# Kernel optimization log

Hardware: AMD Instinct MI355X
Metric: run time of the kernel (lower is better)

The kernel has to match this reference:

```python
import jax, jax.numpy as jnp
import numpy as np

B, S, D, H, DK = 8, 1024, 1024, 16, 64
DV = D // H  # 64


def setup_inputs() -> dict:
    key = jax.random.key(0)
    ks = jax.random.split(key, 9)
    s = 1.0 / np.sqrt(D)
    return {
        "x": jax.random.normal(ks[0], (B, S, D), dtype=jnp.float32),
        "masks": jnp.ones((B, S), dtype=jnp.int32),
        "Wq": jax.random.normal(ks[1], (D, H * DK), dtype=jnp.float32) * s,
        "bq": jnp.zeros((H * DK,), dtype=jnp.float32),
        "Wk": jax.random.normal(ks[2], (D, H * DK), dtype=jnp.float32) * s,
        "bk": jnp.zeros((H * DK,), dtype=jnp.float32),
        "Wv": jax.random.normal(ks[3], (D, H * DV), dtype=jnp.float32) * s,
        "bv": jnp.zeros((H * DV,), dtype=jnp.float32),
        "Wo": jax.random.normal(ks[4], (H * DV, D), dtype=jnp.float32) * s,
        "bo": jnpp_zeros() if False else jnp.zeros((D,), dtype=jnp.float32),
    }


def reference(x, masks, Wq, bq, Wk, bk, Wv, bv, Wo, bo):
    # projections -> [B, H, S, d]
    q = (x @ Wq + bq).reshape(B, S, H, DK).transpose(0, 2, 1, 3)
    k = (x @ Wk + bk).reshape(B, S, H, DK).transpose(0, 2, 1, 3)
    v = (x @ Wv + bv).reshape(B, S, H, DV).transpose(0, 2, 1, 3)
    # scaled dot-product attention with padding mask
    logits = jnp.einsum('bhqd,bhkd->bhqk', q, k) / jnp.sqrt(jnp.float32(DK))
    mask = masks[:, None, None, :]  # [B,1,1,S]
    logits = jnp.where(mask == 0, jnp.float32(-1e9), logits)
    scores = jax.nn.softmax(logits, axis=-1)
    out = jnp.einsum('bhqk,bhkd->bhqd', scores, v)
    out = out.transpose(0, 2, 1, 3).reshape(B, S, H * DV)
    # output projection; dropout is identity in eval mode
    return out @ Wo + bo
```

## Files before the change

### kernel.cpp

```cpp
#include <hip/hip_runtime.h>
#include <stdint.h>

#define B_ 8
#define S_ 1024
#define D_ 1024
#define H_ 16
#define DK_ 64
#define DV_ 64

typedef __attribute__((ext_vector_type(8))) short short8;
typedef __attribute__((ext_vector_type(4))) float f32x4;

__device__ __forceinline__ unsigned short f2bf(float f) {
  union { float f; unsigned u; } v; v.f = f;
  return (unsigned short)((v.u + 0x7fffu + ((v.u >> 16) & 1u)) >> 16);
}
__device__ __forceinline__ unsigned short f2bf_trunc(float f) {
  union { float f; unsigned u; } v; v.f = f;
  return (unsigned short)(v.u >> 16);
}

__device__ __forceinline__ void ld_lds16(const unsigned short* g, unsigned short* l) {
  __builtin_amdgcn_global_load_lds((const __attribute__((address_space(1))) void*)g,
                                   (__attribute__((address_space(3))) void*)l, 16, 0, 0);
}

__global__ __launch_bounds__(256) void prep_kernel(const float* __restrict__ x,
                                                   unsigned short* __restrict__ xb,
                                                   const float* __restrict__ W0,
                                                   const float* __restrict__ W1,
                                                   const float* __restrict__ W2,
                                                   const float* __restrict__ W3,
                                                   unsigned short* __restrict__ T0,
                                                   unsigned short* __restrict__ T1,
                                                   unsigned short* __restrict__ T2,
                                                   unsigned short* __restrict__ T3) {
  const int z = blockIdx.z;
  if (z >= 4) {
    size_t blk = (size_t)(z - 4) * 256 + blockIdx.y * 16 + blockIdx.x;
    size_t i = (blk * 256 + threadIdx.x) * 4;
    float4 v = *(const float4*)(x + i);
    ushort4 o;
    o.x = f2bf(v.x); o.y = f2bf(v.y); o.z = f2bf(v.z); o.w = f2bf(v.w);
    *(ushort4*)(xb + i) = o;
    return;
  }
  __shared__ __align__(16) unsigned short tl[64][65];
  const float* W; unsigned short* Wt;
  switch (z) {
    case 0: W = W0; Wt = T0; break;
    case 1: W = W1; Wt = T1; break;
    case 2: W = W2; Wt = T2; break;
    default: W = W3; Wt = T3; break;
  }
  const int xx = threadIdx.x & 63;
  const int y4 = threadIdx.x >> 6;
  const int bn = blockIdx.x * 64;
  const int bk = blockIdx.y * 64;
  #pragma unroll
  for (int r = y4; r < 64; r += 4)
    tl[r][xx] = f2bf(W[(size_t)(bk + r) * 1024 + bn + xx]);
  __syncthreads();
  #pragma unroll
  for (int r = y4; r < 64; r += 4)
    Wt[(size_t)(bn + r) * 1024 + bk + xx] = tl[xx][r];
}


struct SJob { const unsigned short* g; unsigned short* l; };

__device__ __forceinline__ void stage128(const unsigned short* __restrict__ G,
                                         unsigned short* __restrict__ L, int t) {
  #pragma unroll
  for (int i = 0; i < 2; i++) {
    int s = i * 512 + t;
    int r = s >> 3, cb = s & 7;
    int c = cb ^ (r & 7);
    ld_lds16(G + (size_t)r * 1024 + c * 8, L + (size_t)s * 8);
  }
}

template <bool SW>
__device__ __forceinline__ f32x4 MM(short8 a, short8 b, f32x4 c) {
  if constexpr (SW) return __builtin_amdgcn_mfma_f32_16x16x32_bf16(b, a, c, 0, 0, 0);
  else              return __builtin_amdgcn_mfma_f32_16x16x32_bf16(a, b, c, 0, 0, 0);
}

template <bool SW, int VM>
__device__ __forceinline__ void ktile2(const unsigned short* __restrict__ As_,
                                       const unsigned short* __restrict__ Bs_,
                                       f32x4 (&acc)[4][4],
                                       SJob a0, SJob a1, SJob b2,
                                       int t, int wm, int wn, int l15, int quad, int l7) {
  const int cb0 = (quad ^ l7) * 8;
  const int cb1 = ((4 | quad) ^ l7) * 8;
  short8 af[4], bf[4];

  #pragma unroll
  for (int mi = 0; mi < 4; mi++)
    af[mi] = *(const short8*)&As_[(wm + mi * 16 + l15) * 64 + cb0];
  #pragma unroll
  for (int ni = 0; ni < 4; ni++)
    bf[ni] = *(const short8*)&Bs_[(wn + ni * 16 + l15) * 64 + cb0];
  if (a0.g) stage128(a0.g, a0.l, t);
  if (a1.g) stage128(a1.g, a1.l, t);
  __builtin_amdgcn_s_barrier();
  asm volatile("s_waitcnt lgkmcnt(0)" ::: "memory");
  __builtin_amdgcn_s_setprio(1);
  #pragma unroll
  for (int mi = 0; mi < 4; mi++)
    #pragma unroll
    for (int ni = 0; ni < 4; ni++)
      acc[mi][ni] = MM<SW>(af[mi], bf[ni], acc[mi][ni]);
  __builtin_amdgcn_s_setprio(0);
  __builtin_amdgcn_s_barrier();

  #pragma unroll
  for (int mi = 0; mi < 4; mi++)
    af[mi] = *(const short8*)&As_[(wm + mi * 16 + l15) * 64 + cb1];
  #pragma unroll
  for (int ni = 0; ni < 4; ni++)
    bf[ni] = *(const short8*)&Bs_[(wn + ni * 16 + l15) * 64 + cb1];
  if (b2.g) stage128(b2.g, b2.l, t);
  __builtin_amdgcn_s_barrier();
  asm volatile("s_waitcnt lgkmcnt(0)" ::: "memory");
  __builtin_amdgcn_s_setprio(1);
  #pragma unroll
  for (int mi = 0; mi < 4; mi++)
    #pragma unroll
    for (int ni = 0; ni < 4; ni++)
      acc[mi][ni] = MM<SW>(af[mi], bf[ni], acc[mi][ni]);
  __builtin_amdgcn_s_setprio(0);
  if constexpr (VM == 6) asm volatile("s_waitcnt vmcnt(6)" ::: "memory");
  if constexpr (VM == 0) asm volatile("s_waitcnt vmcnt(0)" ::: "memory");
  __builtin_amdgcn_s_barrier();
}

template <bool SW>
__device__ __forceinline__ void gemm_core(const unsigned short* __restrict__ Ag,
                                          const unsigned short* __restrict__ Bg,
                                          unsigned short* __restrict__ Asl,
                                          unsigned short* __restrict__ Bsl,
                                          f32x4 (&acc)[4][4],
                                          int t, int wm, int wn, int l15, int quad, int l7) {
  unsigned short* A0 = Asl;
  unsigned short* A1 = Asl + 16384;
  unsigned short* A2 = Asl + 32768;
  unsigned short* Bs0 = Bsl;
  unsigned short* Bs1 = Bsl + 8192;
  unsigned short* Bs2 = Bsl + 16384;

  stage128(Ag,                 A0, t);
  stage128(Ag + 128 * 1024,    A0 + 8192, t);
  stage128(Bg,                 Bs0, t);
  stage128(Ag + 64,                A1, t);
  stage128(Ag + 64 + 128 * 1024,   A1 + 8192, t);
  stage128(Bg + 64,                Bs1, t);
  asm volatile("s_waitcnt vmcnt(6)" ::: "memory");
  __builtin_amdgcn_s_barrier();

  #pragma unroll 1
  for (int J = 0; J < 12; J += 3) {
    const unsigned short* Aj = Ag + (size_t)J * 64;
    const unsigned short* Bj = Bg + (size_t)J * 64;
    ktile2<SW, 6>(A0, Bs0, acc,
                  SJob{Aj + 2 * 64, A2}, SJob{Aj + 2 * 64 + 128 * 1024, A2 + 8192},
                  SJob{Bj + 2 * 64, Bs2}, t, wm, wn, l15, quad, l7);
    ktile2<SW, 6>(A1, Bs1, acc,
                  SJob{Aj + 3 * 64, A0}, SJob{Aj + 3 * 64 + 128 * 1024, A0 + 8192},
                  SJob{Bj + 3 * 64, Bs0}, t, wm, wn, l15, quad, l7);
    ktile2<SW, 6>(A2, Bs2, acc,
                  SJob{Aj + 4 * 64, A1}, SJob{Aj + 4 * 64 + 128 * 1024, A1 + 8192},
                  SJob{Bj + 4 * 64, Bs1}, t, wm, wn, l15, quad, l7);
  }
  ktile2<SW, 6>(A0, Bs0, acc,
                SJob{Ag + 14 * 64, A2}, SJob{Ag + 14 * 64 + 128 * 1024, A2 + 8192},
                SJob{Bg + 14 * 64, Bs2}, t, wm, wn, l15, quad, l7);
  ktile2<SW, 6>(A1, Bs1, acc,
                SJob{Ag + 15 * 64, A0}, SJob{Ag + 15 * 64 + 128 * 1024, A0 + 8192},
                SJob{Bg + 15 * 64, Bs0}, t, wm, wn, l15, quad, l7);
  ktile2<SW, 0>(A2, Bs2, acc,
                SJob{nullptr, nullptr}, SJob{nullptr, nullptr}, SJob{nullptr, nullptr},
                t, wm, wn, l15, quad, l7);
  ktile2<SW, -1>(A0, Bs0, acc,
                 SJob{nullptr, nullptr}, SJob{nullptr, nullptr}, SJob{nullptr, nullptr},
                 t, wm, wn, l15, quad, l7);
}

__global__ __launch_bounds__(512, 2) void gemm_qkv8(const unsigned short* __restrict__ A,
                                                    const unsigned short* __restrict__ Bt,
                                                    const float* __restrict__ bq,
                                                    const float* __restrict__ bk,
                                                    const float* __restrict__ bv,
                                                    const int* __restrict__ masks,
                                                    unsigned short* __restrict__ q,
                                                    unsigned short* __restrict__ kk,
                                                    unsigned short* __restrict__ vT) {
  extern __shared__ unsigned short lds[];
  unsigned short* Asl = lds;
  unsigned short* Bsl = lds + 3 * 16384;
  const int t = threadIdx.x;
  const int w = t >> 6, lane = t & 63;
  const int l15 = lane & 15, quad = lane >> 4, l7 = l15 & 7;
  const int lin = blockIdx.y * 24 + blockIdx.x;
  const int lin2 = (lin & 7) * 96 + (lin >> 3);
  const int bxi = lin2 % 24, byi = lin2 / 24;
  const int bm = byi * 256, bn = bxi * 128;
  const int wm = (w >> 1) * 64, wn = (w & 1) * 64;
  const bool vsec = (bxi >= 16);
  const unsigned short* Ag = A + (size_t)bm * 1024;
  const unsigned short* Bg = Bt + (size_t)bn * 1024;

  f32x4 acc[4][4] = {};
  if (!vsec) gemm_core<false>(Ag, Bg, Asl, Bsl, acc, t, wm, wn, l15, quad, l7);
  else       gemm_core<true >(Ag, Bg, Asl, Bsl, acc, t, wm, wn, l15, quad, l7);

  if (!vsec) {
    int sec = bxi >> 3;
    const float* bsel = (sec == 0) ? bq : bk;
    unsigned short* dst = (sec == 0) ? q : kk;
    float scale = (sec == 0) ? 0.180336880f : 1.0f;
    #pragma unroll
    for (int ni = 0; ni < 4; ni++) {
      int c = (bn & 1023) + wn + ni * 16 + l15;
      float bvv = bsel[c];
      int hh = c >> 6, d = c & 63;
      #pragma unroll
      for (int mi = 0; mi < 4; mi++) {
        int row0 = bm + wm + mi * 16 + quad * 4;
        #pragma unroll
        for (int r = 0; r < 4; r++) {
          int row = row0 + r;
          int b = row >> 10, s = row & 1023;
          dst[(((size_t)(b * H_ + hh)) * S_ + s) * DK_ + d] = f2bf((acc[mi][ni][r] + bvv) * scale);
        }
      }
    }
  } else {
    #pragma unroll
    for (int ni = 0; ni < 4; ni++) {
      int cbase = (bn & 1023) + wn + ni * 16;
      #pragma unroll
      for (int mi = 0; mi < 4; mi++) {
        int row = bm + wm + mi * 16 + l15;
        int b = row >> 10, s = row & 1023;
        float mf = (masks[b * S_ + s] != 0) ? 1.0f : 0.0f;
        #pragma unroll
        for (int r = 0; r < 4; r++) {
          int c = cbase + quad * 4 + r;
          int hh = c >> 6, d = c & 63;
          vT[(((size_t)(b * H_ + hh)) * DV_ + d) * S_ + s] = f2bf((acc[mi][ni][r] + bv[c]) * mf);
        }
      }
    }
  }
}

__global__ __launch_bounds__(512, 2) void gemm_out8(const unsigned short* __restrict__ A,
                                                    const unsigned short* __restrict__ Bt,
                                                    const float* __restrict__ bias,
                                                    float* __restrict__ Cout) {
  extern __shared__ unsigned short lds[];
  unsigned short* Asl = lds;
  unsigned short* Bsl = lds + 3 * 16384;
  const int t = threadIdx.x;
  const int w = t >> 6, lane = t & 63;
  const int l15 = lane & 15, quad = lane >> 4, l7 = l15 & 7;
  const int lin = blockIdx.y * 8 + blockIdx.x;
  const int lin2 = (lin & 7) * 32 + (lin >> 3);
  const int bxi = lin2 % 8, byi = lin2 / 8;
  const int bm = byi * 256, bn = bxi * 128;
  const int wm = (w >> 1) * 64, wn = (w & 1) * 64;
  const unsigned short* Ag = A + (size_t)bm * 1024;
  const unsigned short* Bg = Bt + (size_t)bn * 1024;

  f32x4 acc[4][4] = {};
  gemm_core<false>(Ag, Bg, Asl, Bsl, acc, t, wm, wn, l15, quad, l7);

  #pragma unroll
  for (int ni = 0; ni < 4; ni++) {
    int col = bn + wn + ni * 16 + l15;
    float bvv = bias[col];
    #pragma unroll
    for (int mi = 0; mi < 4; mi++) {
      int row0 = bm + wm + mi * 16 + quad * 4;
      #pragma unroll
      for (int r = 0; r < 4; r++)
        Cout[(size_t)(row0 + r) * 1024 + col] = acc[mi][ni][r] + bvv;
    }
  }
}

#define PLD 72
#define VROWS 65
__global__ __launch_bounds__(256) void attn_kernel(const unsigned short* __restrict__ Q,
                                                   const unsigned short* __restrict__ Kb,
                                                   const unsigned short* __restrict__ Vt,
                                                   const int* __restrict__ masks,
                                                   unsigned short* __restrict__ O) {
  __shared__ __align__(16) unsigned short Pl[128 * PLD];
  __shared__ __align__(16) unsigned short Ks[2 * 64 * 64];
  __shared__ __align__(16) unsigned short Vs[(2 * VROWS + 15) * 64];
  const int t = threadIdx.x;
  const int wave = t >> 6, lane = t & 63;
  const int l15 = lane & 15, quad = lane >> 4;
  const int l7 = l15 & 7;
  const int bh = blockIdx.x;
  const int qt = blockIdx.y;
  const int b = bh >> 4, h = bh & 15;

  const unsigned short* Qg = Q + ((size_t)bh * S_ + qt * 128) * DK_;
  const unsigned short* Kg = Kb + (size_t)bh * S_ * DK_;
  const unsigned short* Vg = Vt + (size_t)bh * DV_ * S_;
  const int wslot = (t & ~63);

  int mv[4];
  #pragma unroll
  for (int j = 0; j < 4; j++)
    mv[j] = masks[b * S_ + (j * 4 + wave) * 64 + lane];

  short8 aq[2][2];
  #pragma unroll
  for (int mb = 0; mb < 2; mb++)
    #pragma unroll
    for (int kf = 0; kf < 2; kf++)
      aq[mb][kf] = *(const short8*)(Qg + (size_t)(wave * 32 + mb * 16 + l15) * 64 + kf * 32 + quad * 8);

  auto stage = [&](int kt, int buf) {
    const unsigned short* Kt = Kg + (size_t)kt * 64 * DK_;
    unsigned short* Kd = &Ks[buf * 4096];
    unsigned short* Vd = &Vs[buf * (VROWS * 64)];
    #pragma unroll
    for (int i = 0; i < 2; i++) {
      int p = i * 256 + t;
      int rk = p >> 3, ck = (p & 7) ^ (rk & 7);
      ld_lds16(Kt + (size_t)rk * DK_ + ck * 8, &Kd[(i * 256 + wslot) * 8]);
      ld_lds16(Vg + (size_t)rk * S_ + kt * 64 + ck * 8, &Vd[(i * 256 + wslot) * 8]);
    }
    if (wave == (kt & 3))
      Vd[64 * 64 + lane] = (mv[kt >> 2] != 0) ? (unsigned short)0x3F80 : (unsigned short)0;
  };

  f32x4 o_acc[2][5] = {};

  stage(0, 0);
  __syncthreads();

  #pragma unroll 2
  for (int kt = 0; kt < 16; kt++) {
    const int cur = kt & 1;
    if (kt < 15) stage(kt + 1, cur ^ 1);
    const unsigned short* Kc = &Ks[cur * 4096];
    const unsigned short* Vc = &Vs[cur * (VROWS * 64)];

    f32x4 sc[2][4];
    #pragma unroll
    for (int n = 0; n < 4; n++) {
      short8 bk0 = *(const short8*)&Kc[(n * 16 + l15) * 64 + (quad ^ l7) * 8];
      short8 bk1 = *(const short8*)&Kc[(n * 16 + l15) * 64 + ((4 + quad) ^ l7) * 8];
      #pragma unroll
      for (int mb = 0; mb < 2; mb++) {
        f32x4 c = {};
        c = __builtin_amdgcn_mfma_f32_16x16x32_bf16(bk0, aq[mb][0], c, 0, 0, 0);
        c = __builtin_amdgcn_mfma_f32_16x16x32_bf16(bk1, aq[mb][1], c, 0, 0, 0);
        sc[mb][n] = c;
      }
    }
    #pragma unroll
    for (int mb = 0; mb < 2; mb++)
      #pragma unroll
      for (int n = 0; n < 4; n++) {
        ushort4 pk;
        pk.x = f2bf_trunc(__builtin_amdgcn_exp2f(sc[mb][n][0]));
        pk.y = f2bf_trunc(__builtin_amdgcn_exp2f(sc[mb][n][1]));
        pk.z = f2bf_trunc(__builtin_amdgcn_exp2f(sc[mb][n][2]));
        pk.w = f2bf_trunc(__builtin_amdgcn_exp2f(sc[mb][n][3]));
        *(ushort4*)&Pl[(wave * 32 + mb * 16 + l15) * PLD + n * 16 + quad * 4] = pk;
      }
    #pragma unroll
    for (int kf = 0; kf < 2; kf++) {
      short8 ap[2];
      #pragma unroll
      for (int mb = 0; mb < 2; mb++)
        ap[mb] = *(const short8*)&Pl[(wave * 32 + mb * 16 + l15) * PLD + kf * 32 + quad * 8];
      #pragma unroll
      for (int n = 0; n < 5; n++) {
        short8 bv = *(const short8*)&Vc[(n * 16 + l15) * 64 + ((kf * 4 + quad) ^ l7) * 8];
        #pragma unroll
        for (int mb = 0; mb < 2; mb++)
          o_acc[mb][n] = __builtin_amdgcn_mfma_f32_16x16x32_bf16(ap[mb], bv, o_acc[mb][n], 0, 0, 0);
      }
    }
    __syncthreads();
  }

  #pragma unroll
  for (int mb = 0; mb < 2; mb++)
    #pragma unroll
    for (int r = 0; r < 4; r++) {
      float l = __shfl(o_acc[mb][4][r], lane & 48, 64);
      float inv = __builtin_amdgcn_rcpf(l);
      int qrow = qt * 128 + wave * 32 + mb * 16 + quad * 4 + r;
      #pragma unroll
      for (int n = 0; n < 4; n++) {
        int col = h * 64 + n * 16 + l15;
        O[((size_t)b * S_ + qrow) * D_ + col] = f2bf(o_acc[mb][n][r] * inv);
      }
    }
}

extern "C" void kernel_launch(void* const* d_in, const int* in_sizes, int n_in,
                              void* d_out, int out_size, void* d_ws, size_t ws_size,
                              hipStream_t stream) {
  (void)in_sizes; (void)n_in; (void)out_size; (void)ws_size;
  const float* x  = (const float*)d_in[0];
  const int* masks = (const int*)d_in[1];
  const float* Wq = (const float*)d_in[2];
  const float* bq = (const float*)d_in[3];
  const float* Wk = (const float*)d_in[4];
  const float* bk = (const float*)d_in[5];
  const float* Wv = (const float*)d_in[6];
  const float* bv = (const float*)d_in[7];
  const float* Wo = (const float*)d_in[8];
  const float* bo = (const float*)d_in[9];

  char* p = (char*)d_ws;
  unsigned short* xb    = (unsigned short*)p; p += (size_t)8192 * 1024 * 2;
  unsigned short* WqkvT = (unsigned short*)p; p += (size_t)3072 * 1024 * 2;
  unsigned short* WoT   = (unsigned short*)p; p += (size_t)1024 * 1024 * 2;
  unsigned short* q     = (unsigned short*)p; p += (size_t)8192 * 1024 * 2;
  unsigned short* kk    = (unsigned short*)p; p += (size_t)8192 * 1024 * 2;
  unsigned short* vT    = (unsigned short*)p; p += (size_t)8192 * 1024 * 2;
  unsigned short* at    = (unsigned short*)p; p += (size_t)8192 * 1024 * 2;

  static bool attr_done = false;
  if (!attr_done) {
    hipFuncSetAttribute((const void*)gemm_qkv8, hipFuncAttributeMaxDynamicSharedMemorySize, 147456);
    hipFuncSetAttribute((const void*)gemm_out8, hipFuncAttributeMaxDynamicSharedMemorySize, 147456);
    attr_done = true;
  }

  prep_kernel<<<dim3(16, 16, 36), 256, 0, stream>>>(
      x, xb, Wq, Wk, Wv, Wo,
      WqkvT, WqkvT + (size_t)1024 * 1024, WqkvT + (size_t)2048 * 1024, WoT);
  gemm_qkv8<<<dim3(24, 32), 512, 147456, stream>>>(xb, WqkvT, bq, bk, bv, masks, q, kk, vT);
  attn_kernel<<<dim3(128, 8), 256, 0, stream>>>(q, kk, vT, masks, at);
  gemm_out8<<<dim3(8, 32), 512, 147456, stream>>>(at, WoT, bo, (float*)d_out);
}
```

Before: 249.3 us.

## Use 256x256 tiles with double-buffered pipeline for QKV projection GEMM

Replaces the QKV GEMM's 256x128 tile with a 256x256 tile per block, with eight waves each computing 128x64. It uses a two-stage LDS double buffer and interleaves the global-to-LDS staging into four MFMA sub-phases, with barriers and priority hints between them. The larger tile raises arithmetic intensity and halves the block count (384 blocks), reducing redundant A/B loads. In exchange it needs more accumulator registers at two blocks per CU, exposes more load latency with only two buffers, and drops the block-index swizzle for L2 locality in both GEMMs.

```diff
diff --git a/kernel.cpp b/kernel.cpp
--- a/kernel.cpp
+++ b/kernel.cpp
@@ -66,7 +66,6 @@
     Wt[(size_t)(bn + r) * 1024 + bk + xx] = tl[xx][r];
 }
 
-
 struct SJob { const unsigned short* g; unsigned short* l; };
 
 __device__ __forceinline__ void stage128(const unsigned short* __restrict__ G,
@@ -84,6 +83,208 @@
 __device__ __forceinline__ f32x4 MM(short8 a, short8 b, f32x4 c) {
   if constexpr (SW) return __builtin_amdgcn_mfma_f32_16x16x32_bf16(b, a, c, 0, 0, 0);
   else              return __builtin_amdgcn_mfma_f32_16x16x32_bf16(a, b, c, 0, 0, 0);
+}
+
+template <bool SW, int VM>
+__device__ __forceinline__ void ktile256(const unsigned short* __restrict__ As_,
+                                         const unsigned short* __restrict__ Bs_,
+                                         f32x4 (&acc)[8][4],
+                                         SJob sA0, SJob sA1, SJob sB0, SJob sB1,
+                                         int t, int wm, int wn, int l15, int quad, int l7) {
+  const int cb0 = (quad ^ l7) * 8;
+  const int cb1 = ((4 | quad) ^ l7) * 8;
+  short8 bh0[4], bh1[4];
+  short8 a0, a1, a2, a3;
+
+  #pragma unroll
+  for (int ni = 0; ni < 4; ni++) {
+    bh0[ni] = *(const short8*)&Bs_[(wn + ni * 16 + l15) * 64 + cb0];
+    bh1[ni] = *(const short8*)&Bs_[(wn + ni * 16 + l15) * 64 + cb1];
+  }
+  a0 = *(const short8*)&As_[(wm + 0 * 16 + l15) * 64 + cb0];
+  a1 = *(const short8*)&As_[(wm + 0 * 16 + l15) * 64 + cb1];
+  a2 = *(const short8*)&As_[(wm + 1 * 16 + l15) * 64 + cb0];
+  a3 = *(const short8*)&As_[(wm + 1 * 16 + l15) * 64 + cb1];
+  if (sA0.g) stage128(sA0.g, sA0.l, t);
+  __builtin_amdgcn_s_barrier();
+  asm volatile("s_waitcnt lgkmcnt(0)" ::: "memory");
+  __builtin_amdgcn_s_setprio(1);
+  #pragma unroll
+  for (int ni = 0; ni < 4; ni++) {
+    acc[0][ni] = MM<SW>(a0, bh0[ni], acc[0][ni]);
+    acc[0][ni] = MM<SW>(a1, bh1[ni], acc[0][ni]);
+    acc[1][ni] = MM<SW>(a2, bh0[ni], acc[1][ni]);
+    acc[1][ni] = MM<SW>(a3, bh1[ni], acc[1][ni]);
+  }
+  __builtin_amdgcn_s_setprio(0);
+  __builtin_amdgcn_s_barrier();
+
+  a0 = *(const short8*)&As_[(wm + 2 * 16 + l15) * 64 + cb0];
+  a1 = *(const short8*)&As_[(wm + 2 * 16 + l15) * 64 + cb1];
+  a2 = *(const short8*)&As_[(wm + 3 * 16 + l15) * 64 + cb0];
+  a3 = *(const short8*)&As_[(wm + 3 * 16 + l15) * 64 + cb1];
+  if (sA1.g) stage128(sA1.g, sA1.l, t);
+  __builtin_amdgcn_s_barrier();
+  asm volatile("s_waitcnt lgkmcnt(0)" ::: "memory");
+  __builtin_amdgcn_s_setprio(1);
+  #pragma unroll
+  for (int ni = 0; ni < 4; ni++) {
+    acc[2][ni] = MM<SW>(a0, bh0[ni], acc[2][ni]);
+    acc[2][ni] = MM<SW>(a1, bh1[ni], acc[2][ni]);
+    acc[3][ni] = MM<SW>(a2, bh0[ni], acc[3][ni]);
+    acc[3][ni] = MM<SW>(a3, bh1[ni], acc[3][ni]);
+  }
+  __builtin_amdgcn_s_setprio(0);
+  __builtin_amdgcn_s_barrier();
+
+  a0 = *(const short8*)&As_[(wm + 4 * 16 + l15) * 64 + cb0];
+  a1 = *(const short8*)&As_[(wm + 4 * 16 + l15) * 64 + cb1];
+  a2 = *(const short8*)&As_[(wm + 5 * 16 + l15) * 64 + cb0];
+  a3 = *(const short8*)&As_[(wm + 5 * 16 + l15) * 64 + cb1];
+  if (sB0.g) stage128(sB0.g, sB0.l, t);
+  __builtin_amdgcn_s_barrier();
+  asm volatile("s_waitcnt lgkmcnt(0)" ::: "memory");
+  __builtin_amdgcn_s_setprio(1);
+  #pragma unroll
+  for (int ni = 0; ni < 4; ni++) {
+    acc[4][ni] = MM<SW>(a0, bh0[ni], acc[4][ni]);
+    acc[4][ni] = MM<SW>(a1, bh1[ni], acc[4][ni]);
+    acc[5][ni] = MM<SW>(a2, bh0[ni], acc[5][ni]);
+    acc[5][ni] = MM<SW>(a3, bh1[ni], acc[5][ni]);
+  }
+  __builtin_amdgcn_s_setprio(0);
+  __builtin_amdgcn_s_barrier();
+
+  a0 = *(const short8*)&As_[(wm + 6 * 16 + l15) * 64 + cb0];
+  a1 = *(const short8*)&As_[(wm + 6 * 16 + l15) * 64 + cb1];
+  a2 = *(const short8*)&As_[(wm + 7 * 16 + l15) * 64 + cb0];
+  a3 = *(const short8*)&As_[(wm + 7 * 16 + l15) * 64 + cb1];
+  if (sB1.g) stage128(sB1.g, sB1.l, t);
+  __builtin_amdgcn_s_barrier();
+  asm volatile("s_waitcnt lgkmcnt(0)" ::: "memory");
+  __builtin_amdgcn_s_setprio(1);
+  #pragma unroll
+  for (int ni = 0; ni < 4; ni++) {
+    acc[6][ni] = MM<SW>(a0, bh0[ni], acc[6][ni]);
+    acc[6][ni] = MM<SW>(a1, bh1[ni], acc[6][ni]);
+    acc[7][ni] = MM<SW>(a2, bh0[ni], acc[7][ni]);
+    acc[7][ni] = MM<SW>(a3, bh1[ni], acc[7][ni]);
+  }
+  __builtin_amdgcn_s_setprio(0);
+  if constexpr (VM == 4) asm volatile("s_waitcnt vmcnt(4)" ::: "memory");
+  if constexpr (VM == 0) asm volatile("s_waitcnt vmcnt(0)" ::: "memory");
+  __builtin_amdgcn_s_barrier();
+}
+
+template <bool SW>
+__device__ __forceinline__ void gemm_core256(const unsigned short* __restrict__ Ag,
+                                             const unsigned short* __restrict__ Bg,
+                                             unsigned short* __restrict__ Asl,
+                                             unsigned short* __restrict__ Bsl,
+                                             f32x4 (&acc)[8][4],
+                                             int t, int wm, int wn, int l15, int quad, int l7) {
+  unsigned short* A0 = Asl;
+  unsigned short* A1 = Asl + 16384;
+  unsigned short* B0s = Bsl;
+  unsigned short* B1s = Bsl + 16384;
+
+  stage128(Ag,              A0, t);
+  stage128(Ag + 128 * 1024, A0 + 8192, t);
+  stage128(Bg,              B0s, t);
+  stage128(Bg + 128 * 1024, B0s + 8192, t);
+  stage128(Bg + 64,              B1s, t);
+  stage128(Bg + 64 + 128 * 1024, B1s + 8192, t);
+  asm volatile("s_waitcnt vmcnt(4)" ::: "memory");
+  __builtin_amdgcn_s_barrier();
+
+  #pragma unroll 1
+  for (int J = 0; J < 14; J += 2) {
+    const unsigned short* Aj = Ag + (size_t)J * 64;
+    const unsigned short* Bj = Bg + (size_t)J * 64;
+    ktile256<SW, 4>(A0, B0s, acc,
+                    SJob{Aj + 64, A1}, SJob{Aj + 64 + 128 * 1024, A1 + 8192},
+                    SJob{Bj + 128, B0s}, SJob{Bj + 128 + 128 * 1024, B0s + 8192},
+                    t, wm, wn, l15, quad, l7);
+    ktile256<SW, 4>(A1, B1s, acc,
+                    SJob{Aj + 128, A0}, SJob{Aj + 128 + 128 * 1024, A0 + 8192},
+                    SJob{Bj + 192, B1s}, SJob{Bj + 192 + 128 * 1024, B1s + 8192},
+                    t, wm, wn, l15, quad, l7);
+  }
+  ktile256<SW, 0>(A0, B0s, acc,
+                  SJob{Ag + 15 * 64, A1}, SJob{Ag + 15 * 64 + 128 * 1024, A1 + 8192},
+                  SJob{nullptr, nullptr}, SJob{nullptr, nullptr},
+                  t, wm, wn, l15, quad, l7);
+  ktile256<SW, -1>(A1, B1s, acc,
+                   SJob{nullptr, nullptr}, SJob{nullptr, nullptr},
+                   SJob{nullptr, nullptr}, SJob{nullptr, nullptr},
+                   t, wm, wn, l15, quad, l7);
+}
+
+__global__ __launch_bounds__(512, 2) void gemm_qkv8(const unsigned short* __restrict__ A,
+                                                    const unsigned short* __restrict__ Bt,
+                                                    const float* __restrict__ bq,
+                                                    const float* __restrict__ bk,
+                                                    const float* __restrict__ bv,
+                                                    const int* __restrict__ masks,
+                                                    unsigned short* __restrict__ q,
+                                                    unsigned short* __restrict__ kk,
+                                                    unsigned short* __restrict__ vT) {
+  extern __shared__ unsigned short lds[];
+  unsigned short* Asl = lds;
+  unsigned short* Bsl = lds + 2 * 16384;
+  const int t = threadIdx.x;
+  const int w = t >> 6, lane = t & 63;
+  const int l15 = lane & 15, quad = lane >> 4, l7 = l15 & 7;
+  const int bxi = blockIdx.x, byi = blockIdx.y;
+  const int bm = byi * 256, bn = bxi * 256;
+  const int wm = (w >> 2) * 128, wn = (w & 3) * 64;
+  const bool vsec = (bxi >= 8);
+  const unsigned short* Ag = A + (size_t)bm * 1024;
+  const unsigned short* Bg = Bt + (size_t)bn * 1024;
+
+  f32x4 acc[8][4] = {};
+  if (!vsec) gemm_core256<false>(Ag, Bg, Asl, Bsl, acc, t, wm, wn, l15, quad, l7);
+  else       gemm_core256<true >(Ag, Bg, Asl, Bsl, acc, t, wm, wn, l15, quad, l7);
+
+  if (!vsec) {
+    int sec = bxi >> 2;
+    const float* bsel = (sec == 0) ? bq : bk;
+    unsigned short* dst = (sec == 0) ? q : kk;
+    float scale = (sec == 0) ? 0.180336880f : 1.0f;
+    #pragma unroll
+    for (int ni = 0; ni < 4; ni++) {
+      int c = (bxi & 3) * 256 + wn + ni * 16 + l15;
+      float bvv = bsel[c];
+      int hh = c >> 6, d = c & 63;
+      #pragma unroll
+      for (int mi = 0; mi < 8; mi++) {
+        int row0 = bm + wm + mi * 16 + quad * 4;
+        #pragma unroll
+        for (int r = 0; r < 4; r++) {
+          int row = row0 + r;
+          int b = row >> 10, s = row & 1023;
+          dst[(((size_t)(b * H_ + hh)) * S_ + s) * DK_ + d] = f2bf((acc[mi][ni][r] + bvv) * scale);
+        }
+      }
+    }
+  } else {
+    #pragma unroll
+    for (int ni = 0; ni < 4; ni++) {
+      int cbase = (bxi & 3) * 256 + wn + ni * 16;
+      #pragma unroll
+      for (int mi = 0; mi < 8; mi++) {
+        int row = bm + wm + mi * 16 + l15;
+        int b = row >> 10, s = row & 1023;
+        float mf = (masks[b * S_ + s] != 0) ? 1.0f : 0.0f;
+        #pragma unroll
+        for (int r = 0; r < 4; r++) {
+          int c = cbase + quad * 4 + r;
+          int hh = c >> 6, d = c & 63;
+          vT[(((size_t)(b * H_ + hh)) * DV_ + d) * S_ + s] = f2bf((acc[mi][ni][r] + bv[c]) * mf);
+        }
+      }
+    }
+  }
 }
 
 template <bool SW, int VM>
@@ -187,75 +388,6 @@
                  t, wm, wn, l15, quad, l7);
 }
 
-__global__ __launch_bounds__(512, 2) void gemm_qkv8(const unsigned short* __restrict__ A,
-                                                    const unsigned short* __restrict__ Bt,
-                                                    const float* __restrict__ bq,
-                                                    const float* __restrict__ bk,
-                                                    const float* __restrict__ bv,
-                                                    const int* __restrict__ masks,
-                                                    unsigned short* __restrict__ q,
-                                                    unsigned short* __restrict__ kk,
-                                                    unsigned short* __restrict__ vT) {
-  extern __shared__ unsigned short lds[];
-  unsigned short* Asl = lds;
-  unsigned short* Bsl = lds + 3 * 16384;
-  const int t = threadIdx.x;
-  const int w = t >> 6, lane = t & 63;
-  const int l15 = lane & 15, quad = lane >> 4, l7 = l15 & 7;
-  const int lin = blockIdx.y * 24 + blockIdx.x;
-  const int lin2 = (lin & 7) * 96 + (lin >> 3);
-  const int bxi = lin2 % 24, byi = lin2 / 24;
-  const int bm = byi * 256, bn = bxi * 128;
-  const int wm = (w >> 1) * 64, wn = (w & 1) * 64;
-  const bool vsec = (bxi >= 16);
-  const unsigned short* Ag = A + (size_t)bm * 1024;
-  const unsigned short* Bg = Bt + (size_t)bn * 1024;
-
-  f32x4 acc[4][4] = {};
-  if (!vsec) gemm_core<false>(Ag, Bg, Asl, Bsl, acc, t, wm, wn, l15, quad, l7);
-  else       gemm_core<true >(Ag, Bg, Asl, Bsl, acc, t, wm, wn, l15, quad, l7);
-
-  if (!vsec) {
-    int sec = bxi >> 3;
-    const float* bsel = (sec == 0) ? bq : bk;
-    unsigned short* dst = (sec == 0) ? q : kk;
-    float scale = (sec == 0) ? 0.180336880f : 1.0f;
-    #pragma unroll
-    for (int ni = 0; ni < 4; ni++) {
-      int c = (bn & 1023) + wn + ni * 16 + l15;
-      float bvv = bsel[c];
-      int hh = c >> 6, d = c & 63;
-      #pragma unroll
-      for (int mi = 0; mi < 4; mi++) {
-        int row0 = bm + wm + mi * 16 + quad * 4;
-        #pragma unroll
-        for (int r = 0; r < 4; r++) {
-          int row = row0 + r;
-          int b = row >> 10, s = row & 1023;
-          dst[(((size_t)(b * H_ + hh)) * S_ + s) * DK_ + d] = f2bf((acc[mi][ni][r] + bvv) * scale);
-        }
-      }
-    }
-  } else {
-    #pragma unroll
-    for (int ni = 0; ni < 4; ni++) {
-      int cbase = (bn & 1023) + wn + ni * 16;
-      #pragma unroll
-      for (int mi = 0; mi < 4; mi++) {
-        int row = bm + wm + mi * 16 + l15;
-        int b = row >> 10, s = row & 1023;
-        float mf = (masks[b * S_ + s] != 0) ? 1.0f : 0.0f;
-        #pragma unroll
-        for (int r = 0; r < 4; r++) {
-          int c = cbase + quad * 4 + r;
-          int hh = c >> 6, d = c & 63;
-          vT[(((size_t)(b * H_ + hh)) * DV_ + d) * S_ + s] = f2bf((acc[mi][ni][r] + bv[c]) * mf);
-        }
-      }
-    }
-  }
-}
-
 __global__ __launch_bounds__(512, 2) void gemm_out8(const unsigned short* __restrict__ A,
                                                     const unsigned short* __restrict__ Bt,
                                                     const float* __restrict__ bias,
@@ -266,10 +398,7 @@
   const int t = threadIdx.x;
   const int w = t >> 6, lane = t & 63;
   const int l15 = lane & 15, quad = lane >> 4, l7 = l15 & 7;
-  const int lin = blockIdx.y * 8 + blockIdx.x;
-  const int lin2 = (lin & 7) * 32 + (lin >> 3);
-  const int bxi = lin2 % 8, byi = lin2 / 8;
-  const int bm = byi * 256, bn = bxi * 128;
+  const int bm = blockIdx.y * 256, bn = blockIdx.x * 128;
   const int wm = (w >> 1) * 64, wn = (w & 1) * 64;
   const unsigned short* Ag = A + (size_t)bm * 1024;
   const unsigned short* Bg = Bt + (size_t)bn * 1024;
@@ -435,7 +564,7 @@
 
   static bool attr_done = false;
   if (!attr_done) {
-    hipFuncSetAttribute((const void*)gemm_qkv8, hipFuncAttributeMaxDynamicSharedMemorySize, 147456);
+    hipFuncSetAttribute((const void*)gemm_qkv8, hipFuncAttributeMaxDynamicSharedMemorySize, 131072);
     hipFuncSetAttribute((const void*)gemm_out8, hipFuncAttributeMaxDynamicSharedMemorySize, 147456);
     attr_done = true;
   }
@@ -443,7 +572,7 @@
   prep_kernel<<<dim3(16, 16, 36), 256, 0, stream>>>(
       x, xb, Wq, Wk, Wv, Wo,
       WqkvT, WqkvT + (size_t)1024 * 1024, WqkvT + (size_t)2048 * 1024, WoT);
-  gemm_qkv8<<<dim3(24, 32), 512, 147456, stream>>>(xb, WqkvT, bq, bk, bv, masks, q, kk, vT);
+  gemm_qkv8<<<dim3(12, 32), 512, 131072, stream>>>(xb, WqkvT, bq, bk, bv, masks, q, kk, vT);
   attn_kernel<<<dim3(128, 8), 256, 0, stream>>>(q, kk, vT, masks, at);
   gemm_out8<<<dim3(8, 32), 512, 147456, stream>>>(at, WoT, bo, (float*)d_out);
 }
```

Result: no change. 253.0 us (+1.5%).
